# Optimization experiments

Hardware: AMD Instinct MI355X
Metric: run time of the kernel (lower is better)

The kernel has to match this reference:

```python
import jax, jax.numpy as jnp
import numpy as np

B, N, C = 128, 196, 2048   # batch, regions (14x14), conv channels
H, A = 512, 512            # hidden_size, attention_size


def setup_inputs() -> dict:
    key = jax.random.key(0)
    ks = jax.random.split(key, 10)
    s = lambda d: 1.0 / np.sqrt(d)
    return {
        "img_embedding": jax.random.normal(ks[0], (B, N, C), jnp.float32),
        "hidden": jax.random.normal(ks[1], (B, H), jnp.float32),
        "W_img": jax.random.uniform(ks[2], (C, A), jnp.float32, -s(C), s(C)),
        "b_img": jax.random.uniform(ks[3], (A,), jnp.float32, -s(C), s(C)),
        "W_hid": jax.random.uniform(ks[4], (H, A), jnp.float32, -s(H), s(H)),
        "b_hid": jax.random.uniform(ks[5], (A,), jnp.float32, -s(H), s(H)),
        "w_att": jax.random.uniform(ks[6], (A,), jnp.float32, -s(A), s(A)),
        "b_att": jax.random.uniform(ks[7], (), jnp.float32, -s(A), s(A)),
        "w_beta": jax.random.uniform(ks[8], (H,), jnp.float32, -s(H), s(H)),
        "b_beta": jax.random.uniform(ks[9], (), jnp.float32, -s(H), s(H)),
    }


def reference(img_embedding, hidden, W_img, b_img, W_hid, b_hid,
              w_att, b_att, w_beta, b_beta):
    # img_embedding: (B, N, C); hidden: (B, H)
    img_att = jnp.einsum('bnc,ca->bna', img_embedding, W_img) + b_img   # (B,N,A)
    hid_att = hidden @ W_hid + b_hid                                    # (B,A)
    # additive attention scores -> (B, N)
    scores = jnp.einsum('bna,a->bn',
                        jax.nn.relu(img_att + hid_att[:, None, :]), w_att) + b_att
    beta = jax.nn.sigmoid(hidden @ w_beta + b_beta)                     # (B,)
    attention_weights = jax.nn.softmax(scores, axis=-1)                 # (B,N)
    context = beta[:, None] * jnp.einsum('bn,bnc->bc',
                                         attention_weights, img_embedding)  # (B,C)
    return context, attention_weights
```

## Files before the change

kernel.cpp:

```cpp
#include <hip/hip_runtime.h>
#include <hip/hip_bf16.h>
#include <math.h>

typedef __bf16 bf16v8 __attribute__((ext_vector_type(8)));
typedef float  f32x4  __attribute__((ext_vector_type(4)));

__device__ __forceinline__ void gload_lds16(const void* g, void* l) {
    __builtin_amdgcn_global_load_lds(
        (const __attribute__((address_space(1))) unsigned int*)g,
        (__attribute__((address_space(3))) unsigned int*)l, 16, 0, 0);
}

__global__ __launch_bounds__(256) void wt_k(const float* __restrict__ W,
                                            unsigned short* __restrict__ Wt)
{
    __shared__ float tile[64][65];
    const int k0 = blockIdx.x * 64;
    const int a0 = blockIdx.y * 64;
    const int t = threadIdx.x;
    const int c = t & 63, rbase = t >> 6;
#pragma unroll
    for (int i = 0; i < 16; ++i) {
        int kr = rbase + i * 4;
        tile[kr][c] = W[(k0 + kr) * 512 + a0 + c];
    }
    __syncthreads();
#pragma unroll
    for (int i = 0; i < 16; ++i) {
        int ar = rbase + i * 4;
        Wt[(a0 + ar) * 2048 + k0 + c] =
            __builtin_bit_cast(unsigned short, (__bf16)tile[c][ar]);
    }
}

__global__ __launch_bounds__(256) void hid_k(
    const float* __restrict__ hidden, const float* __restrict__ W_hid,
    const float* __restrict__ b_hid,  const float* __restrict__ b_img,
    const float* __restrict__ w_beta, const float* __restrict__ b_beta,
    float* __restrict__ hb, float* __restrict__ betap)
{
    const int b = blockIdx.x, t = threadIdx.x;
    __shared__ float hs[512];
    __shared__ float red[4];
    hs[t]       = hidden[b * 512 + t];
    hs[t + 256] = hidden[b * 512 + 256 + t];
    __syncthreads();
    float a0 = 0.f, a1 = 0.f;
#pragma unroll 4
    for (int h = 0; h < 512; ++h) {
        float hv = hs[h];
        a0 = fmaf(hv, W_hid[h * 512 + t], a0);
        a1 = fmaf(hv, W_hid[h * 512 + 256 + t], a1);
    }
    hb[b * 512 + t]       = a0 + b_hid[t]       + b_img[t];
    hb[b * 512 + 256 + t] = a1 + b_hid[256 + t] + b_img[256 + t];

    float x = hs[t] * w_beta[t] + hs[t + 256] * w_beta[t + 256];
#pragma unroll
    for (int k = 32; k >= 1; k >>= 1) x += __shfl_xor(x, k, 64);
    const int lane = t & 63, wid = t >> 6;
    if (lane == 0) red[wid] = x;
    __syncthreads();
    if (t == 0) {
        float s = red[0] + red[1] + red[2] + red[3] + b_beta[0];
        betap[b] = 1.f / (1.f + __expf(-s));
    }
}

#define NKIT 64

__global__ __launch_bounds__(256) void scores_gemm(
    const float* __restrict__ img,
    const unsigned short* __restrict__ Wt,
    const float* __restrict__ hb,
    const float* __restrict__ w_att,
    float* __restrict__ partials)
{
    __shared__ __align__(16) char smem[49152];
    char* As = smem;
    char* Bs = smem + 32768;

    const int tid  = threadIdx.x;
    const int lane = tid & 63;
    const int wid  = tid >> 6;
    const int wm   = wid >> 1;
    const int wn   = wid & 1;

    const int id = blockIdx.x;
    const int wg = (id & 7) * 98 + (id >> 3);
    const int cb    = wg & 3;
    const int mtile = wg >> 2;
    const int r0 = mtile * 128;
    const int a0 = cb * 128;

    const float* gA[4];
#pragma unroll
    for (int r = 0; r < 4; ++r) {
        int row = (wid * 4 + r) * 8 + (lane >> 3);
        gA[r] = img + (size_t)(r0 + row) * 2048 + (((lane & 7) ^ (lane >> 3)) << 2);
    }
    const unsigned short* gB[2];
#pragma unroll
    for (int r = 0; r < 2; ++r) {
        int col = (wid * 2 + r) * 16 + (lane >> 2);
        gB[r] = Wt + (size_t)(a0 + col) * 2048 +
                (((lane & 3) ^ ((lane >> 2) & 3)) << 3);
    }

    const int g  = lane >> 4;
    const int fl = lane & 15;

    f32x4 acc[4][4] = {};

    {
        char* asn = As + (wid * 4) * 1024;
        char* bsn = Bs + (wid * 2) * 1024;
#pragma unroll
        for (int r = 0; r < 4; ++r) gload_lds16(gA[r], asn + r * 1024);
#pragma unroll
        for (int r = 0; r < 2; ++r) gload_lds16(gB[r], bsn + r * 1024);
    }
    __syncthreads();

    for (int it = 0; it < NKIT; ++it) {
        const int bsel = it & 1;
        if (it + 1 < NKIT) {
            char* asn = As + (bsel ^ 1) * 16384 + (wid * 4) * 1024;
            char* bsn = Bs + (bsel ^ 1) * 8192  + (wid * 2) * 1024;
#pragma unroll
            for (int r = 0; r < 4; ++r)
                gload_lds16(gA[r] + (it + 1) * 32, asn + r * 1024);
#pragma unroll
            for (int r = 0; r < 2; ++r)
                gload_lds16(gB[r] + (it + 1) * 32, bsn + r * 1024);
        }

        char* asw = As + bsel * 16384;
        char* bsw = Bs + bsel * 8192;

        bf16v8 av[4], bv[4];
#pragma unroll
        for (int fm = 0; fm < 4; ++fm) {
            int row = wm * 64 + fm * 16 + fl;
            const char* pa = asw + row * 128;
            int sw = (fl & 7) << 4;
            f32x4 lo = *(const f32x4*)(pa + ((g * 32) ^ sw));
            f32x4 hi = *(const f32x4*)(pa + ((g * 32 + 16) ^ sw));
            bf16v8 a;
            a[0] = (__bf16)lo[0]; a[1] = (__bf16)lo[1];
            a[2] = (__bf16)lo[2]; a[3] = (__bf16)lo[3];
            a[4] = (__bf16)hi[0]; a[5] = (__bf16)hi[1];
            a[6] = (__bf16)hi[2]; a[7] = (__bf16)hi[3];
            av[fm] = a;
        }
#pragma unroll
        for (int fn = 0; fn < 4; ++fn) {
            int col = wn * 64 + fn * 16 + fl;
            bv[fn] = *(const bf16v8*)(bsw + col * 64 + ((g * 16) ^ ((fl & 3) << 4)));
        }
#pragma unroll
        for (int fm = 0; fm < 4; ++fm)
#pragma unroll
            for (int fn = 0; fn < 4; ++fn)
                acc[fm][fn] = __builtin_amdgcn_mfma_f32_16x16x32_bf16(
                    av[fm], bv[fn], acc[fm][fn], 0, 0, 0);

        __syncthreads();
    }

    float* red = (float*)smem;
    const int l4 = lane >> 4;

    float w4[4];
#pragma unroll
    for (int fn = 0; fn < 4; ++fn) w4[fn] = w_att[a0 + wn * 64 + fn * 16 + fl];

#pragma unroll
    for (int fm = 0; fm < 4; ++fm) {
#pragma unroll
        for (int rg = 0; rg < 4; ++rg) {
            int row = wm * 64 + fm * 16 + l4 * 4 + rg;
            int grow = r0 + row;
            int bb = grow / 196;
            const float* hbrow = hb + bb * 512 + a0 + wn * 64;
            float s = 0.f;
#pragma unroll
            for (int fn = 0; fn < 4; ++fn) {
                float v = acc[fm][fn][rg] + hbrow[fn * 16 + fl];
                v = fmaxf(v, 0.f);
                s = fmaf(v, w4[fn], s);
            }
#pragma unroll
            for (int m = 1; m < 16; m <<= 1) s += __shfl_xor(s, m, 64);
            if (fl == 0) red[wn * 128 + row] = s;
        }
    }
    __syncthreads();
    if (tid < 128) {
        partials[cb * 25088 + r0 + tid] = red[tid] + red[128 + tid];
    }
}

__global__ __launch_bounds__(256) void softmax_k(
    const float* __restrict__ partials, const float* __restrict__ betap,
    const float* __restrict__ b_att,
    float* __restrict__ out_w, float* __restrict__ wbeta)
{
    const int b = blockIdx.x;
    const int t = threadIdx.x;
    const int lane = t & 63, wid = t >> 6;
    __shared__ float red[4];

    float scv = 0.f, sc = -1e30f;
    if (t < 196) {
        int r = b * 196 + t;
        scv = partials[r] + partials[25088 + r] + partials[2 * 25088 + r] +
              partials[3 * 25088 + r] + b_att[0];
        sc = scv;
    }
    float m = sc;
#pragma unroll
    for (int k = 32; k >= 1; k >>= 1) m = fmaxf(m, __shfl_xor(m, k, 64));
    if (lane == 0) red[wid] = m;
    __syncthreads();
    m = fmaxf(fmaxf(red[0], red[1]), fmaxf(red[2], red[3]));

    float e = (t < 196) ? __expf(scv - m) : 0.f;
    float ssum = e;
#pragma unroll
    for (int k = 32; k >= 1; k >>= 1) ssum += __shfl_xor(ssum, k, 64);
    __syncthreads();
    if (lane == 0) red[wid] = ssum;
    __syncthreads();
    float denom = red[0] + red[1] + red[2] + red[3];

    if (t < 196) {
        float w = e / denom;
        out_w[b * 196 + t] = w;
        wbeta[b * 196 + t] = w * betap[b];
    }
}

__global__ __launch_bounds__(256) void ctx_k(
    const float* __restrict__ img, const float* __restrict__ wbeta,
    float* __restrict__ out)
{
    const int b = blockIdx.y;
    const int c0 = blockIdx.x * 512 + threadIdx.x * 2;
    __shared__ float w[200];
    if (threadIdx.x < 196) w[threadIdx.x] = wbeta[b * 196 + threadIdx.x];
    __syncthreads();
    const float* base = img + (size_t)b * 196 * 2048 + c0;
    float acx = 0.f, acy = 0.f;
#pragma unroll 4
    for (int n = 0; n < 196; ++n) {
        float2 v = *(const float2*)(base + (size_t)n * 2048);
        float wn = w[n];
        acx = fmaf(wn, v.x, acx);
        acy = fmaf(wn, v.y, acy);
    }
    float2 r; r.x = acx; r.y = acy;
    *(float2*)(out + b * 2048 + c0) = r;
}

extern "C" void kernel_launch(void* const* d_in, const int* in_sizes, int n_in,
                              void* d_out, int out_size, void* d_ws, size_t ws_size,
                              hipStream_t stream)
{
    const float* img    = (const float*)d_in[0];
    const float* hidden = (const float*)d_in[1];
    const float* W_img  = (const float*)d_in[2];
    const float* b_img  = (const float*)d_in[3];
    const float* W_hid  = (const float*)d_in[4];
    const float* b_hid  = (const float*)d_in[5];
    const float* w_att  = (const float*)d_in[6];
    const float* b_att  = (const float*)d_in[7];
    const float* w_beta = (const float*)d_in[8];
    const float* b_beta = (const float*)d_in[9];

    char* ws = (char*)d_ws;
    unsigned short* Wt = (unsigned short*)ws;
    float* hbp   = (float*)(ws + 2097152);
    float* betap = (float*)(ws + 2359296);
    float* parts = (float*)(ws + 2359808);
    float* wbeta = (float*)(ws + 2761216);

    float* out_ctx = (float*)d_out;
    float* out_w   = out_ctx + 128 * 2048;

    wt_k<<<dim3(32, 8), 256, 0, stream>>>(W_img, Wt);
    hid_k<<<128, 256, 0, stream>>>(hidden, W_hid, b_hid, b_img, w_beta, b_beta,
                                   hbp, betap);
    scores_gemm<<<784, 256, 0, stream>>>(img, Wt, hbp, w_att, parts);
    softmax_k<<<128, 256, 0, stream>>>(parts, betap, b_att, out_w, wbeta);
    ctx_k<<<dim3(4, 128), 256, 0, stream>>>(img, wbeta, out_ctx);
}
```

Baseline: 195.1 us.

## Stage image tile through registers and convert to bf16 before LDS store

The A operand (fp32 image rows) now goes into registers with float4 loads, is converted to bf16 once, and is stored into a padded bf16 LDS tile. Before, fp32 went straight to LDS and every wave converted it on each read. This halves A's LDS footprint, cuts shared memory from 48KB to 36KB, and launch bounds now request 3 blocks per CU. The prefetch is restructured into a manually unrolled two-stage ping-pong with register-held A data, which adds VGPR pressure and moves the conversion cost onto the store path.

```diff
diff --git a/kernel.cpp b/kernel.cpp
--- a/kernel.cpp
+++ b/kernel.cpp
@@ -9,6 +9,17 @@
     __builtin_amdgcn_global_load_lds(
         (const __attribute__((address_space(1))) unsigned int*)g,
         (__attribute__((address_space(3))) unsigned int*)l, 16, 0, 0);
+}
+
+__device__ __forceinline__ void cvt_store(void* dst, float4 a, float4 b,
+                                          float4 c, float4 d) {
+    bf16v8 v0, v1;
+    v0[0] = (__bf16)a.x; v0[1] = (__bf16)a.y; v0[2] = (__bf16)a.z; v0[3] = (__bf16)a.w;
+    v0[4] = (__bf16)b.x; v0[5] = (__bf16)b.y; v0[6] = (__bf16)b.z; v0[7] = (__bf16)b.w;
+    v1[0] = (__bf16)c.x; v1[1] = (__bf16)c.y; v1[2] = (__bf16)c.z; v1[3] = (__bf16)c.w;
+    v1[4] = (__bf16)d.x; v1[5] = (__bf16)d.y; v1[6] = (__bf16)d.z; v1[7] = (__bf16)d.w;
+    *(bf16v8*)dst = v0;
+    *(bf16v8*)((char*)dst + 16) = v1;
 }
 
 __global__ __launch_bounds__(256) void wt_k(const float* __restrict__ W,
@@ -69,16 +80,18 @@
 
 #define NKIT 64
 
-__global__ __launch_bounds__(256) void scores_gemm(
+__global__ __launch_bounds__(256, 3) void scores_gemm(
     const float* __restrict__ img,
     const unsigned short* __restrict__ Wt,
     const float* __restrict__ hb,
     const float* __restrict__ w_att,
     float* __restrict__ partials)
 {
-    __shared__ __align__(16) char smem[49152];
-    char* As = smem;
-    char* Bs = smem + 32768;
+    __shared__ __align__(16) char smem[36864];
+    char* A0 = smem;
+    char* A1 = smem + 10240;
+    char* B0 = smem + 20480;
+    char* B1 = smem + 28672;
 
     const int tid  = threadIdx.x;
     const int lane = tid & 63;
@@ -93,79 +106,96 @@
     const int r0 = mtile * 128;
     const int a0 = cb * 128;
 
-    const float* gA[4];
-#pragma unroll
-    for (int r = 0; r < 4; ++r) {
-        int row = (wid * 4 + r) * 8 + (lane >> 3);
-        gA[r] = img + (size_t)(r0 + row) * 2048 + (((lane & 7) ^ (lane >> 3)) << 2);
-    }
-    const unsigned short* gB[2];
-#pragma unroll
-    for (int r = 0; r < 2; ++r) {
-        int col = (wid * 2 + r) * 16 + (lane >> 2);
-        gB[r] = Wt + (size_t)(a0 + col) * 2048 +
-                (((lane & 3) ^ ((lane >> 2) & 3)) << 3);
-    }
+    const int arow = tid >> 1;
+    const int ah   = tid & 1;
+    const float* gA = img + (size_t)(r0 + arow) * 2048 + ah * 16;
+    const int aW = arow * 80 + ah * 32;
+
+    const int bswz = ((tid & 3) ^ ((tid >> 3) & 3)) * 8;
+    const unsigned short* gB0 = Wt + (size_t)(a0 + (tid >> 2)) * 2048 + bswz;
+    const unsigned short* gB1 = Wt + (size_t)(a0 + 64 + (tid >> 2)) * 2048 + bswz;
+    const int bW0 = tid * 16;
+    const int bW1 = 4096 + tid * 16;
 
     const int g  = lane >> 4;
     const int fl = lane & 15;
 
     f32x4 acc[4][4] = {};
+    float4 rA0[4], rA1[4];
 
     {
-        char* asn = As + (wid * 4) * 1024;
-        char* bsn = Bs + (wid * 2) * 1024;
-#pragma unroll
-        for (int r = 0; r < 4; ++r) gload_lds16(gA[r], asn + r * 1024);
-#pragma unroll
-        for (int r = 0; r < 2; ++r) gload_lds16(gB[r], bsn + r * 1024);
-    }
-    __syncthreads();
-
-    for (int it = 0; it < NKIT; ++it) {
-        const int bsel = it & 1;
-        if (it + 1 < NKIT) {
-            char* asn = As + (bsel ^ 1) * 16384 + (wid * 4) * 1024;
-            char* bsn = Bs + (bsel ^ 1) * 8192  + (wid * 2) * 1024;
-#pragma unroll
-            for (int r = 0; r < 4; ++r)
-                gload_lds16(gA[r] + (it + 1) * 32, asn + r * 1024);
-#pragma unroll
-            for (int r = 0; r < 2; ++r)
-                gload_lds16(gB[r] + (it + 1) * 32, bsn + r * 1024);
+        const float4* p = (const float4*)gA;
+        rA0[0] = p[0]; rA0[1] = p[1]; rA0[2] = p[2]; rA0[3] = p[3];
+    }
+    gload_lds16(gB0, B0 + bW0);
+    gload_lds16(gB1, B0 + bW1);
+    __syncthreads();
+    cvt_store(A0 + aW, rA0[0], rA0[1], rA0[2], rA0[3]);
+    {
+        const float4* p = (const float4*)(gA + 32);
+        rA1[0] = p[0]; rA1[1] = p[1]; rA1[2] = p[2]; rA1[3] = p[3];
+    }
+    __syncthreads();
+
+    for (int t = 0; t < NKIT; t += 2) {
+        {
+            bf16v8 av[4], bv[4];
+#pragma unroll
+            for (int fm = 0; fm < 4; ++fm) {
+                int row = wm * 64 + fm * 16 + fl;
+                av[fm] = *(const bf16v8*)(A0 + row * 80 + g * 16);
+            }
+#pragma unroll
+            for (int fn = 0; fn < 4; ++fn) {
+                int col = wn * 64 + fn * 16 + fl;
+                bv[fn] = *(const bf16v8*)(B0 + col * 64 +
+                                          ((g ^ ((col >> 1) & 3)) << 4));
+            }
+            if (t + 2 < NKIT) {
+                const float4* p = (const float4*)(gA + (t + 2) * 32);
+                rA0[0] = p[0]; rA0[1] = p[1]; rA0[2] = p[2]; rA0[3] = p[3];
+            }
+            gload_lds16(gB0 + (t + 1) * 32, B1 + bW0);
+            gload_lds16(gB1 + (t + 1) * 32, B1 + bW1);
+            cvt_store(A1 + aW, rA1[0], rA1[1], rA1[2], rA1[3]);
+#pragma unroll
+            for (int fm = 0; fm < 4; ++fm)
+#pragma unroll
+                for (int fn = 0; fn < 4; ++fn)
+                    acc[fm][fn] = __builtin_amdgcn_mfma_f32_16x16x32_bf16(
+                        av[fm], bv[fn], acc[fm][fn], 0, 0, 0);
+            __syncthreads();
         }
-
-        char* asw = As + bsel * 16384;
-        char* bsw = Bs + bsel * 8192;
-
-        bf16v8 av[4], bv[4];
-#pragma unroll
-        for (int fm = 0; fm < 4; ++fm) {
-            int row = wm * 64 + fm * 16 + fl;
-            const char* pa = asw + row * 128;
-            int sw = (fl & 7) << 4;
-            f32x4 lo = *(const f32x4*)(pa + ((g * 32) ^ sw));
-            f32x4 hi = *(const f32x4*)(pa + ((g * 32 + 16) ^ sw));
-            bf16v8 a;
-            a[0] = (__bf16)lo[0]; a[1] = (__bf16)lo[1];
-            a[2] = (__bf16)lo[2]; a[3] = (__bf16)lo[3];
-            a[4] = (__bf16)hi[0]; a[5] = (__bf16)hi[1];
-            a[6] = (__bf16)hi[2]; a[7] = (__bf16)hi[3];
-            av[fm] = a;
+        {
+            bf16v8 av[4], bv[4];
+#pragma unroll
+            for (int fm = 0; fm < 4; ++fm) {
+                int row = wm * 64 + fm * 16 + fl;
+                av[fm] = *(const bf16v8*)(A1 + row * 80 + g * 16);
+            }
+#pragma unroll
+            for (int fn = 0; fn < 4; ++fn) {
+                int col = wn * 64 + fn * 16 + fl;
+                bv[fn] = *(const bf16v8*)(B1 + col * 64 +
+                                          ((g ^ ((col >> 1) & 3)) << 4));
+            }
+            if (t + 3 < NKIT) {
+                const float4* p = (const float4*)(gA + (t + 3) * 32);
+                rA1[0] = p[0]; rA1[1] = p[1]; rA1[2] = p[2]; rA1[3] = p[3];
+            }
+            if (t + 2 < NKIT) {
+                gload_lds16(gB0 + (t + 2) * 32, B0 + bW0);
+                gload_lds16(gB1 + (t + 2) * 32, B0 + bW1);
+                cvt_store(A0 + aW, rA0[0], rA0[1], rA0[2], rA0[3]);
+            }
+#pragma unroll
+            for (int fm = 0; fm < 4; ++fm)
+#pragma unroll
+                for (int fn = 0; fn < 4; ++fn)
+                    acc[fm][fn] = __builtin_amdgcn_mfma_f32_16x16x32_bf16(
+                        av[fm], bv[fn], acc[fm][fn], 0, 0, 0);
+            __syncthreads();
         }
-#pragma unroll
-        for (int fn = 0; fn < 4; ++fn) {
-            int col = wn * 64 + fn * 16 + fl;
-            bv[fn] = *(const bf16v8*)(bsw + col * 64 + ((g * 16) ^ ((fl & 3) << 4)));
-        }
-#pragma unroll
-        for (int fm = 0; fm < 4; ++fm)
-#pragma unroll
-            for (int fn = 0; fn < 4; ++fn)
-                acc[fm][fn] = __builtin_amdgcn_mfma_f32_16x16x32_bf16(
-                    av[fm], bv[fn], acc[fm][fn], 0, 0, 0);
-
-        __syncthreads();
     }
 
     float* red = (float*)smem;
```

After: 213.8 us. 1.1x slower.

## Restructure scores GEMM with 64-row tiles and register-staged bf16 A conversion

Applied to the files above, without the earlier changes.

The scores GEMM drops from 128x128 to 64x128 tiles, doubling the grid to 1568 blocks. It now loads fp32 image rows into registers two stages ahead and converts them to bf16 once before writing to LDS, instead of converting in every wave's fragment read. LDS use shrinks to about 26KB with padded rows, and launch bounds request 5 blocks per CU for more occupancy. A hand-unrolled loop with manual waitcnt and barriers overlaps loads with MFMA, at the cost of fragile scheduling and half the B reuse per tile.

```diff
diff --git a/kernel.cpp b/kernel.cpp
--- a/kernel.cpp
+++ b/kernel.cpp
@@ -9,6 +9,13 @@
     __builtin_amdgcn_global_load_lds(
         (const __attribute__((address_space(1))) unsigned int*)g,
         (__attribute__((address_space(3))) unsigned int*)l, 16, 0, 0);
+}
+
+__device__ __forceinline__ void cvt_store8(void* dst, float4 a, float4 b) {
+    bf16v8 v;
+    v[0] = (__bf16)a.x; v[1] = (__bf16)a.y; v[2] = (__bf16)a.z; v[3] = (__bf16)a.w;
+    v[4] = (__bf16)b.x; v[5] = (__bf16)b.y; v[6] = (__bf16)b.z; v[7] = (__bf16)b.w;
+    *(bf16v8*)dst = v;
 }
 
 __global__ __launch_bounds__(256) void wt_k(const float* __restrict__ W,
@@ -69,16 +76,18 @@
 
 #define NKIT 64
 
-__global__ __launch_bounds__(256) void scores_gemm(
+__global__ __launch_bounds__(256, 5) void scores_gemm(
     const float* __restrict__ img,
     const unsigned short* __restrict__ Wt,
     const float* __restrict__ hb,
     const float* __restrict__ w_att,
     float* __restrict__ partials)
 {
-    __shared__ __align__(16) char smem[49152];
-    char* As = smem;
-    char* Bs = smem + 32768;
+    __shared__ __align__(16) char smem[26624];
+    char* A0 = smem;
+    char* A1 = smem + 5120;
+    char* B0 = smem + 10240;
+    char* B1 = smem + 18432;
 
     const int tid  = threadIdx.x;
     const int lane = tid & 63;
@@ -87,86 +96,92 @@
     const int wn   = wid & 1;
 
     const int id = blockIdx.x;
-    const int wg = (id & 7) * 98 + (id >> 3);
+    const int wg = (id & 7) * 196 + (id >> 3);
     const int cb    = wg & 3;
     const int mtile = wg >> 2;
-    const int r0 = mtile * 128;
+    const int r0 = mtile * 64;
     const int a0 = cb * 128;
 
-    const float* gA[4];
-#pragma unroll
-    for (int r = 0; r < 4; ++r) {
-        int row = (wid * 4 + r) * 8 + (lane >> 3);
-        gA[r] = img + (size_t)(r0 + row) * 2048 + (((lane & 7) ^ (lane >> 3)) << 2);
-    }
-    const unsigned short* gB[2];
-#pragma unroll
-    for (int r = 0; r < 2; ++r) {
-        int col = (wid * 2 + r) * 16 + (lane >> 2);
-        gB[r] = Wt + (size_t)(a0 + col) * 2048 +
-                (((lane & 3) ^ ((lane >> 2) & 3)) << 3);
-    }
+    const int arow = tid >> 2;
+    const int aq   = tid & 3;
+    const float* gA = img + (size_t)(r0 + arow) * 2048 + aq * 8;
+    const int aW = arow * 80 + aq * 16;
+
+    const int bswz = ((tid & 3) ^ ((tid >> 3) & 3)) * 8;
+    const unsigned short* gB0 = Wt + (size_t)(a0 + (tid >> 2)) * 2048 + bswz;
+    const unsigned short* gB1 = Wt + (size_t)(a0 + 64 + (tid >> 2)) * 2048 + bswz;
+    const int bW0 = tid * 16;
+    const int bW1 = 4096 + tid * 16;
 
     const int g  = lane >> 4;
     const int fl = lane & 15;
-
-    f32x4 acc[4][4] = {};
-
-    {
-        char* asn = As + (wid * 4) * 1024;
-        char* bsn = Bs + (wid * 2) * 1024;
-#pragma unroll
-        for (int r = 0; r < 4; ++r) gload_lds16(gA[r], asn + r * 1024);
-#pragma unroll
-        for (int r = 0; r < 2; ++r) gload_lds16(gB[r], bsn + r * 1024);
-    }
-    __syncthreads();
-
-    for (int it = 0; it < NKIT; ++it) {
-        const int bsel = it & 1;
-        if (it + 1 < NKIT) {
-            char* asn = As + (bsel ^ 1) * 16384 + (wid * 4) * 1024;
-            char* bsn = Bs + (bsel ^ 1) * 8192  + (wid * 2) * 1024;
-#pragma unroll
-            for (int r = 0; r < 4; ++r)
-                gload_lds16(gA[r] + (it + 1) * 32, asn + r * 1024);
-#pragma unroll
-            for (int r = 0; r < 2; ++r)
-                gload_lds16(gB[r] + (it + 1) * 32, bsn + r * 1024);
-        }
-
-        char* asw = As + bsel * 16384;
-        char* bsw = Bs + bsel * 8192;
-
-        bf16v8 av[4], bv[4];
-#pragma unroll
-        for (int fm = 0; fm < 4; ++fm) {
-            int row = wm * 64 + fm * 16 + fl;
-            const char* pa = asw + row * 128;
-            int sw = (fl & 7) << 4;
-            f32x4 lo = *(const f32x4*)(pa + ((g * 32) ^ sw));
-            f32x4 hi = *(const f32x4*)(pa + ((g * 32 + 16) ^ sw));
-            bf16v8 a;
-            a[0] = (__bf16)lo[0]; a[1] = (__bf16)lo[1];
-            a[2] = (__bf16)lo[2]; a[3] = (__bf16)lo[3];
-            a[4] = (__bf16)hi[0]; a[5] = (__bf16)hi[1];
-            a[6] = (__bf16)hi[2]; a[7] = (__bf16)hi[3];
-            av[fm] = a;
-        }
-#pragma unroll
-        for (int fn = 0; fn < 4; ++fn) {
-            int col = wn * 64 + fn * 16 + fl;
-            bv[fn] = *(const bf16v8*)(bsw + col * 64 + ((g * 16) ^ ((fl & 3) << 4)));
-        }
-#pragma unroll
-        for (int fm = 0; fm < 4; ++fm)
-#pragma unroll
-            for (int fn = 0; fn < 4; ++fn)
-                acc[fm][fn] = __builtin_amdgcn_mfma_f32_16x16x32_bf16(
-                    av[fm], bv[fn], acc[fm][fn], 0, 0, 0);
-
-        __syncthreads();
-    }
+    const int bro = (g ^ ((fl >> 1) & 3)) << 4;
+
+    f32x4 acc[2][4] = {};
+    float4 rA0[2], rA1[2];
+
+    rA0[0] = *(const float4*)(gA);
+    rA0[1] = *(const float4*)(gA + 4);
+    gload_lds16(gB0, B0 + bW0);
+    gload_lds16(gB1, B0 + bW1);
+    __builtin_amdgcn_sched_barrier(0);
+    cvt_store8(A0 + aW, rA0[0], rA0[1]);
+    rA0[0] = *(const float4*)(gA + 32);
+    rA0[1] = *(const float4*)(gA + 36);
+    rA1[0] = *(const float4*)(gA + 64);
+    rA1[1] = *(const float4*)(gA + 68);
+    __syncthreads();
+
+#define BODY(K, CA, CB, NA, NB, RC, STAGE, RELOAD, FULLBAR) do {            \
+    bf16v8 av0, av1, bv0, bv1, bv2, bv3;                                     \
+    {                                                                        \
+        int row0 = wm * 32 + fl;                                             \
+        av0 = *(const bf16v8*)(CA + row0 * 80 + g * 16);                     \
+        av1 = *(const bf16v8*)(CA + (row0 + 16) * 80 + g * 16);              \
+        int c0 = wn * 64 + fl;                                               \
+        bv0 = *(const bf16v8*)(CB + c0 * 64 + bro);                          \
+        bv1 = *(const bf16v8*)(CB + (c0 + 16) * 64 + bro);                   \
+        bv2 = *(const bf16v8*)(CB + (c0 + 32) * 64 + bro);                   \
+        bv3 = *(const bf16v8*)(CB + (c0 + 48) * 64 + bro);                   \
+    }                                                                        \
+    if (STAGE) {                                                             \
+        gload_lds16(gB0 + (K + 1) * 32, NB + bW0);                           \
+        gload_lds16(gB1 + (K + 1) * 32, NB + bW1);                           \
+    }                                                                        \
+    __builtin_amdgcn_sched_barrier(0);                                       \
+    if (STAGE) cvt_store8(NA + aW, RC[0], RC[1]);                            \
+    if (RELOAD) {                                                            \
+        RC[0] = *(const float4*)(gA + (K + 3) * 32);                         \
+        RC[1] = *(const float4*)(gA + (K + 3) * 32 + 4);                     \
+    }                                                                        \
+    __builtin_amdgcn_sched_barrier(0);                                       \
+    acc[0][0] = __builtin_amdgcn_mfma_f32_16x16x32_bf16(av0, bv0, acc[0][0], 0, 0, 0); \
+    acc[0][1] = __builtin_amdgcn_mfma_f32_16x16x32_bf16(av0, bv1, acc[0][1], 0, 0, 0); \
+    acc[0][2] = __builtin_amdgcn_mfma_f32_16x16x32_bf16(av0, bv2, acc[0][2], 0, 0, 0); \
+    acc[0][3] = __builtin_amdgcn_mfma_f32_16x16x32_bf16(av0, bv3, acc[0][3], 0, 0, 0); \
+    acc[1][0] = __builtin_amdgcn_mfma_f32_16x16x32_bf16(av1, bv0, acc[1][0], 0, 0, 0); \
+    acc[1][1] = __builtin_amdgcn_mfma_f32_16x16x32_bf16(av1, bv1, acc[1][1], 0, 0, 0); \
+    acc[1][2] = __builtin_amdgcn_mfma_f32_16x16x32_bf16(av1, bv2, acc[1][2], 0, 0, 0); \
+    acc[1][3] = __builtin_amdgcn_mfma_f32_16x16x32_bf16(av1, bv3, acc[1][3], 0, 0, 0); \
+    if (FULLBAR) {                                                           \
+        __syncthreads();                                                     \
+    } else {                                                                 \
+        __builtin_amdgcn_sched_barrier(0);                                   \
+        asm volatile("s_waitcnt vmcnt(2) lgkmcnt(0)" ::: "memory");          \
+        __builtin_amdgcn_s_barrier();                                        \
+        __builtin_amdgcn_sched_barrier(0);                                   \
+    }                                                                        \
+} while (0)
+
+    for (int t = 0; t < 60; t += 2) {
+        BODY(t,     A0, B0, A1, B1, rA0, true, true, false);
+        BODY(t + 1, A1, B1, A0, B0, rA1, true, true, false);
+    }
+    BODY(60, A0, B0, A1, B1, rA0, true,  true,  true);
+    BODY(61, A1, B1, A0, B0, rA1, true,  false, true);
+    BODY(62, A0, B0, A1, B1, rA0, true,  false, true);
+    BODY(63, A1, B1, A0, B0, rA1, false, false, true);
+#undef BODY
 
     float* red = (float*)smem;
     const int l4 = lane >> 4;
@@ -176,10 +191,10 @@
     for (int fn = 0; fn < 4; ++fn) w4[fn] = w_att[a0 + wn * 64 + fn * 16 + fl];
 
 #pragma unroll
-    for (int fm = 0; fm < 4; ++fm) {
+    for (int fm = 0; fm < 2; ++fm) {
 #pragma unroll
         for (int rg = 0; rg < 4; ++rg) {
-            int row = wm * 64 + fm * 16 + l4 * 4 + rg;
+            int row = wm * 32 + fm * 16 + l4 * 4 + rg;
             int grow = r0 + row;
             int bb = grow / 196;
             const float* hbrow = hb + bb * 512 + a0 + wn * 64;
@@ -192,12 +207,12 @@
             }
 #pragma unroll
             for (int m = 1; m < 16; m <<= 1) s += __shfl_xor(s, m, 64);
-            if (fl == 0) red[wn * 128 + row] = s;
+            if (fl == 0) red[wn * 64 + row] = s;
         }
     }
     __syncthreads();
-    if (tid < 128) {
-        partials[cb * 25088 + r0 + tid] = red[tid] + red[128 + tid];
+    if (tid < 64) {
+        partials[cb * 25088 + r0 + tid] = red[tid] + red[64 + tid];
     }
 }
 
@@ -291,7 +306,7 @@
     wt_k<<<dim3(32, 8), 256, 0, stream>>>(W_img, Wt);
     hid_k<<<128, 256, 0, stream>>>(hidden, W_hid, b_hid, b_img, w_beta, b_beta,
                                    hbp, betap);
-    scores_gemm<<<784, 256, 0, stream>>>(img, Wt, hbp, w_att, parts);
+    scores_gemm<<<1568, 256, 0, stream>>>(img, Wt, hbp, w_att, parts);
     softmax_k<<<128, 256, 0, stream>>>(parts, betap, b_att, out_w, wbeta);
     ctx_k<<<dim3(4, 128), 256, 0, stream>>>(img, wbeta, out_ctx);
 }
```

After: 219.5 us. 1.12x slower.

## Replace LDS-staged scores GEMM with direct global-load MFMA kernel

Applied to the files above, without the earlier changes.

The scores GEMM no longer stages A and B tiles through double-buffered shared memory. Each wave now loads its fp32 image rows and bf16 weight columns straight from global memory into registers, using a 64x128 tile per block and twice as many blocks, and the shared-memory reduction is replaced by direct partial writes. This removes LDS traffic and barriers but gives up reuse across waves, so each weight fragment is fetched by every wave and the global access pattern is less coalesced. Separately, the context kernel switches from float2 to scalar loads with twice as many blocks.

```diff
diff --git a/kernel.cpp b/kernel.cpp
--- a/kernel.cpp
+++ b/kernel.cpp
@@ -4,12 +4,6 @@
 
 typedef __bf16 bf16v8 __attribute__((ext_vector_type(8)));
 typedef float  f32x4  __attribute__((ext_vector_type(4)));
-
-__device__ __forceinline__ void gload_lds16(const void* g, void* l) {
-    __builtin_amdgcn_global_load_lds(
-        (const __attribute__((address_space(1))) unsigned int*)g,
-        (__attribute__((address_space(3))) unsigned int*)l, 16, 0, 0);
-}
 
 __global__ __launch_bounds__(256) void wt_k(const float* __restrict__ W,
                                             unsigned short* __restrict__ Wt)
@@ -67,137 +61,64 @@
     }
 }
 
-#define NKIT 64
-
-__global__ __launch_bounds__(256) void scores_gemm(
+__global__ __launch_bounds__(256, 4) void scores_direct(
     const float* __restrict__ img,
     const unsigned short* __restrict__ Wt,
     const float* __restrict__ hb,
     const float* __restrict__ w_att,
     float* __restrict__ partials)
 {
-    __shared__ __align__(16) char smem[49152];
-    char* As = smem;
-    char* Bs = smem + 32768;
-
     const int tid  = threadIdx.x;
     const int lane = tid & 63;
     const int wid  = tid >> 6;
-    const int wm   = wid >> 1;
-    const int wn   = wid & 1;
+    const int g    = lane >> 4;
+    const int fl   = lane & 15;
 
     const int id = blockIdx.x;
-    const int wg = (id & 7) * 98 + (id >> 3);
-    const int cb    = wg & 3;
+    const int wg = (id & 7) * 196 + (id >> 3);
+    const int nb    = wg & 3;
     const int mtile = wg >> 2;
-    const int r0 = mtile * 128;
-    const int a0 = cb * 128;
-
-    const float* gA[4];
-#pragma unroll
-    for (int r = 0; r < 4; ++r) {
-        int row = (wid * 4 + r) * 8 + (lane >> 3);
-        gA[r] = img + (size_t)(r0 + row) * 2048 + (((lane & 7) ^ (lane >> 3)) << 2);
-    }
-    const unsigned short* gB[2];
-#pragma unroll
-    for (int r = 0; r < 2; ++r) {
-        int col = (wid * 2 + r) * 16 + (lane >> 2);
-        gB[r] = Wt + (size_t)(a0 + col) * 2048 +
-                (((lane & 3) ^ ((lane >> 2) & 3)) << 3);
-    }
-
-    const int g  = lane >> 4;
-    const int fl = lane & 15;
-
-    f32x4 acc[4][4] = {};
-
-    {
-        char* asn = As + (wid * 4) * 1024;
-        char* bsn = Bs + (wid * 2) * 1024;
-#pragma unroll
-        for (int r = 0; r < 4; ++r) gload_lds16(gA[r], asn + r * 1024);
-#pragma unroll
-        for (int r = 0; r < 2; ++r) gload_lds16(gB[r], bsn + r * 1024);
-    }
-    __syncthreads();
-
-    for (int it = 0; it < NKIT; ++it) {
-        const int bsel = it & 1;
-        if (it + 1 < NKIT) {
-            char* asn = As + (bsel ^ 1) * 16384 + (wid * 4) * 1024;
-            char* bsn = Bs + (bsel ^ 1) * 8192  + (wid * 2) * 1024;
-#pragma unroll
-            for (int r = 0; r < 4; ++r)
-                gload_lds16(gA[r] + (it + 1) * 32, asn + r * 1024);
-#pragma unroll
-            for (int r = 0; r < 2; ++r)
-                gload_lds16(gB[r] + (it + 1) * 32, bsn + r * 1024);
+    const int r0 = mtile * 64;
+
+    const float* gA = img + (size_t)(r0 + wid * 16 + fl) * 2048 + g * 8;
+    const unsigned short* gB = Wt + (size_t)(nb * 128 + fl) * 2048 + g * 8;
+
+    f32x4 acc[8] = {};
+
+    for (int it = 0; it < 64; ++it) {
+        float4 a0 = *(const float4*)(gA + it * 32);
+        float4 a1 = *(const float4*)(gA + it * 32 + 4);
+        bf16v8 av;
+        av[0] = (__bf16)a0.x; av[1] = (__bf16)a0.y;
+        av[2] = (__bf16)a0.z; av[3] = (__bf16)a0.w;
+        av[4] = (__bf16)a1.x; av[5] = (__bf16)a1.y;
+        av[6] = (__bf16)a1.z; av[7] = (__bf16)a1.w;
+#pragma unroll
+        for (int fn = 0; fn < 8; ++fn) {
+            bf16v8 bv = *(const bf16v8*)(gB + (size_t)fn * 16 * 2048 + it * 32);
+            acc[fn] = __builtin_amdgcn_mfma_f32_16x16x32_bf16(av, bv, acc[fn],
+                                                              0, 0, 0);
         }
-
-        char* asw = As + bsel * 16384;
-        char* bsw = Bs + bsel * 8192;
-
-        bf16v8 av[4], bv[4];
-#pragma unroll
-        for (int fm = 0; fm < 4; ++fm) {
-            int row = wm * 64 + fm * 16 + fl;
-            const char* pa = asw + row * 128;
-            int sw = (fl & 7) << 4;
-            f32x4 lo = *(const f32x4*)(pa + ((g * 32) ^ sw));
-            f32x4 hi = *(const f32x4*)(pa + ((g * 32 + 16) ^ sw));
-            bf16v8 a;
-            a[0] = (__bf16)lo[0]; a[1] = (__bf16)lo[1];
-            a[2] = (__bf16)lo[2]; a[3] = (__bf16)lo[3];
-            a[4] = (__bf16)hi[0]; a[5] = (__bf16)hi[1];
-            a[6] = (__bf16)hi[2]; a[7] = (__bf16)hi[3];
-            av[fm] = a;
+    }
+
+    float w4[8];
+#pragma unroll
+    for (int fn = 0; fn < 8; ++fn) w4[fn] = w_att[nb * 128 + fn * 16 + fl];
+
+#pragma unroll
+    for (int rg = 0; rg < 4; ++rg) {
+        int growC = r0 + wid * 16 + g * 4 + rg;
+        const float* hbrow = hb + (growC / 196) * 512 + nb * 128;
+        float s = 0.f;
+#pragma unroll
+        for (int fn = 0; fn < 8; ++fn) {
+            float v = acc[fn][rg] + hbrow[fn * 16 + fl];
+            v = fmaxf(v, 0.f);
+            s = fmaf(v, w4[fn], s);
         }
 #pragma unroll
-        for (int fn = 0; fn < 4; ++fn) {
-            int col = wn * 64 + fn * 16 + fl;
-            bv[fn] = *(const bf16v8*)(bsw + col * 64 + ((g * 16) ^ ((fl & 3) << 4)));
-        }
-#pragma unroll
-        for (int fm = 0; fm < 4; ++fm)
-#pragma unroll
-            for (int fn = 0; fn < 4; ++fn)
-                acc[fm][fn] = __builtin_amdgcn_mfma_f32_16x16x32_bf16(
-                    av[fm], bv[fn], acc[fm][fn], 0, 0, 0);
-
-        __syncthreads();
-    }
-
-    float* red = (float*)smem;
-    const int l4 = lane >> 4;
-
-    float w4[4];
-#pragma unroll
-    for (int fn = 0; fn < 4; ++fn) w4[fn] = w_att[a0 + wn * 64 + fn * 16 + fl];
-
-#pragma unroll
-    for (int fm = 0; fm < 4; ++fm) {
-#pragma unroll
-        for (int rg = 0; rg < 4; ++rg) {
-            int row = wm * 64 + fm * 16 + l4 * 4 + rg;
-            int grow = r0 + row;
-            int bb = grow / 196;
-            const float* hbrow = hb + bb * 512 + a0 + wn * 64;
-            float s = 0.f;
-#pragma unroll
-            for (int fn = 0; fn < 4; ++fn) {
-                float v = acc[fm][fn][rg] + hbrow[fn * 16 + fl];
-                v = fmaxf(v, 0.f);
-                s = fmaf(v, w4[fn], s);
-            }
-#pragma unroll
-            for (int m = 1; m < 16; m <<= 1) s += __shfl_xor(s, m, 64);
-            if (fl == 0) red[wn * 128 + row] = s;
-        }
-    }
-    __syncthreads();
-    if (tid < 128) {
-        partials[cb * 25088 + r0 + tid] = red[tid] + red[128 + tid];
+        for (int m = 1; m < 16; m <<= 1) s += __shfl_xor(s, m, 64);
+        if (fl == 0) partials[nb * 25088 + growC] = s;
     }
 }
 
@@ -246,21 +167,17 @@
     float* __restrict__ out)
 {
     const int b = blockIdx.y;
-    const int c0 = blockIdx.x * 512 + threadIdx.x * 2;
+    const int c0 = blockIdx.x * 256 + threadIdx.x;
     __shared__ float w[200];
     if (threadIdx.x < 196) w[threadIdx.x] = wbeta[b * 196 + threadIdx.x];
     __syncthreads();
     const float* base = img + (size_t)b * 196 * 2048 + c0;
-    float acx = 0.f, acy = 0.f;
+    float acc = 0.f;
 #pragma unroll 4
     for (int n = 0; n < 196; ++n) {
-        float2 v = *(const float2*)(base + (size_t)n * 2048);
-        float wn = w[n];
-        acx = fmaf(wn, v.x, acx);
-        acy = fmaf(wn, v.y, acy);
-    }
-    float2 r; r.x = acx; r.y = acy;
-    *(float2*)(out + b * 2048 + c0) = r;
+        acc = fmaf(w[n], base[(size_t)n * 2048], acc);
+    }
+    out[b * 2048 + c0] = acc;
 }
 
 extern "C" void kernel_launch(void* const* d_in, const int* in_sizes, int n_in,
@@ -291,7 +208,7 @@
     wt_k<<<dim3(32, 8), 256, 0, stream>>>(W_img, Wt);
     hid_k<<<128, 256, 0, stream>>>(hidden, W_hid, b_hid, b_img, w_beta, b_beta,
                                    hbp, betap);
-    scores_gemm<<<784, 256, 0, stream>>>(img, Wt, hbp, w_att, parts);
+    scores_direct<<<1568, 256, 0, stream>>>(img, Wt, hbp, w_att, parts);
     softmax_k<<<128, 256, 0, stream>>>(parts, betap, b_att, out_w, wbeta);
-    ctx_k<<<dim3(4, 128), 256, 0, stream>>>(img, wbeta, out_ctx);
-}
+    ctx_k<<<dim3(8, 128), 256, 0, stream>>>(img, wbeta, out_ctx);
+}
```

New measurement: 594.5 us. 205% more time.
